# Kernel tuning notes

Measured on AMD Instinct MI355X. Metric: run time of the kernel, lower is better.

## Reference

```python
import jax, jax.numpy as jnp
import numpy as np

DIM = 2048
HEADS = 16
DIM_HEAD = 128
DIM_INNER = HEADS * DIM_HEAD
BATCH = 2
SEQ = 2048
EPS = 1e-12  # F.normalize default eps


def l2norm(t, axis=-1):
    # matches F.normalize(t, dim=axis, p=2): t / max(||t||, eps)
    n = jnp.sqrt(jnp.sum(t * t, axis=axis, keepdims=True))
    return t / jnp.maximum(n, EPS)


def setup_inputs() -> dict:
    key = jax.random.key(0)
    ks = jax.random.split(key, 5)
    x = jax.random.normal(ks[0], (BATCH, SEQ, DIM), dtype=jnp.float32)
    # NormLinear weights (torch Linear layout: [out, in]); parametrization
    # l2-normalizes rows (dim=-1) for q/k/v and columns (dim=0) for to_out.
    Wq = jax.random.normal(ks[1], (DIM_INNER, DIM), dtype=jnp.float32) / np.sqrt(DIM)
    Wk = jax.random.normal(ks[2], (DIM_INNER, DIM), dtype=jnp.float32) / np.sqrt(DIM)
    Wv = jax.random.normal(ks[3], (DIM_INNER, DIM), dtype=jnp.float32) / np.sqrt(DIM)
    Wout = jax.random.normal(ks[4], (DIM, DIM_INNER), dtype=jnp.float32) / np.sqrt(DIM_INNER)
    # Scale(dim_inner, init=1.0, scale=dim**-1): param = ones * dim**-1,
    # forward_scale = init/scale = dim, so qk_scale() starts at 1.0
    qk_scale = jnp.ones((DIM_INNER,), dtype=jnp.float32) / DIM
    return {"x": x, "Wq": Wq, "Wk": Wk, "Wv": Wv, "Wout": Wout, "qk_scale": qk_scale}


def reference(x, Wq, Wk, Wv, Wout, qk_scale):
    b, n, _ = x.shape
    # NormLinear: x @ l2norm(W, rows).T  (scale = groups**-1 = 1)
    q = jnp.einsum('bnd,ed->bne', x, l2norm(Wq, axis=-1))
    k = jnp.einsum('bnd,ed->bne', x, l2norm(Wk, axis=-1))
    v = jnp.einsum('bnd,ed->bne', x, l2norm(Wv, axis=-1))
    # split heads: b n (h d) -> b h n d
    split = lambda t: t.reshape(b, n, HEADS, DIM_HEAD).transpose(0, 2, 1, 3)
    q, k, v = split(q), split(k), split(v)
    # per-head l2norm of q and k over head dim
    q = l2norm(q, axis=-1)
    k = l2norm(k, axis=-1)
    # learned qk scale: (h d) -> h 1 d, effective = param * forward_scale(=DIM)
    q = q * (qk_scale * DIM).reshape(HEADS, 1, DIM_HEAD)
    # causal SDPA with scale = sqrt(dim_head) (unit-norm q,k in nGPT)
    attn_scale = DIM_HEAD ** 0.5
    scores = jnp.einsum('bhid,bhjd->bhij', q, k) * attn_scale
    causal = jnp.tril(jnp.ones((n, n), dtype=bool))
    scores = jnp.where(causal, scores, jnp.finfo(scores.dtype).min)
    attn = jax.nn.softmax(scores, axis=-1)
    out = jnp.einsum('bhij,bhjd->bhid', attn, v)
    # merge heads: b h n d -> b n (h d)
    out = out.transpose(0, 2, 1, 3).reshape(b, n, DIM_INNER)
    # to_out: NormLinear with norm over dim=0 of weight [DIM, DIM_INNER]
    out = jnp.einsum('bne,de->bnd', out, l2norm(Wout, axis=0))
    return out
```

## Files before the change

kernel.cpp:

```cpp
#include <hip/hip_runtime.h>


typedef __bf16 bf16x8 __attribute__((ext_vector_type(8)));
typedef float f32x4 __attribute__((ext_vector_type(4)));

__device__ __forceinline__ unsigned short f2bf(float f) {
  unsigned int u = __float_as_uint(f);
  u = u + 0x7FFFu + ((u >> 16) & 1u);
  return (unsigned short)(u >> 16);
}

__device__ __forceinline__ void async16(const void* g, void* l) {
  __builtin_amdgcn_global_load_lds(
      (const __attribute__((address_space(1))) unsigned int*)g,
      (__attribute__((address_space(3))) unsigned int*)l, 16, 0, 0);
}

#define QFOLD (2048.0f * 11.313708498984761f * 1.4426950408889634f)


__global__ __launch_bounds__(256) void prep_w_rows(
    const float* __restrict__ Wq, const float* __restrict__ Wk,
    const float* __restrict__ Wv, ushort* __restrict__ oq,
    ushort* __restrict__ ok_, ushort* __restrict__ ov) {
  const int row = blockIdx.x;
  const float* W = (blockIdx.y == 0) ? Wq : (blockIdx.y == 1) ? Wk : Wv;
  ushort* O = (blockIdx.y == 0) ? oq : (blockIdx.y == 1) ? ok_ : ov;
  const int t = threadIdx.x;
  const float4* Wr = (const float4*)(W + (size_t)row * 2048);
  float4 v0 = Wr[t];
  float4 v1 = Wr[t + 256];
  float ss = v0.x * v0.x + v0.y * v0.y + v0.z * v0.z + v0.w * v0.w +
             v1.x * v1.x + v1.y * v1.y + v1.z * v1.z + v1.w * v1.w;
  ss += __shfl_xor(ss, 1);  ss += __shfl_xor(ss, 2);
  ss += __shfl_xor(ss, 4);  ss += __shfl_xor(ss, 8);
  ss += __shfl_xor(ss, 16); ss += __shfl_xor(ss, 32);
  __shared__ float red[4];
  if ((t & 63) == 0) red[t >> 6] = ss;
  __syncthreads();
  float tot = red[0] + red[1] + red[2] + red[3];
  float sc = 1.0f / fmaxf(sqrtf(tot), 1e-12f);
  ushort4 o0, o1;
  o0.x = f2bf(v0.x * sc); o0.y = f2bf(v0.y * sc);
  o0.z = f2bf(v0.z * sc); o0.w = f2bf(v0.w * sc);
  o1.x = f2bf(v1.x * sc); o1.y = f2bf(v1.y * sc);
  o1.z = f2bf(v1.z * sc); o1.w = f2bf(v1.w * sc);
  *(ushort4*)(O + (size_t)row * 2048 + t * 4) = o0;
  *(ushort4*)(O + (size_t)row * 2048 + 1024 + t * 4) = o1;
}

__global__ __launch_bounds__(256) void wout_colss(const float* __restrict__ W,
                                                  float* __restrict__ colss) {
  const int e = blockIdx.x * 256 + threadIdx.x;
  const int d0 = blockIdx.y * 128;
  float ss = 0.f;
  #pragma unroll 8
  for (int i = 0; i < 128; ++i) {
    float v = W[(size_t)(d0 + i) * 2048 + e];
    ss += v * v;
  }
  atomicAdd(colss + e, ss);
}

__global__ __launch_bounds__(256) void wout_norm(const float* __restrict__ W,
                                                 const float* __restrict__ colss,
                                                 ushort* __restrict__ O) {
  const int idx = (blockIdx.x * 256 + threadIdx.x) * 4;
  float4 v = *(const float4*)(W + idx);
  float4 c = *(const float4*)(colss + (idx & 2047));
  ushort4 o;
  o.x = f2bf(v.x / fmaxf(sqrtf(c.x), 1e-12f));
  o.y = f2bf(v.y / fmaxf(sqrtf(c.y), 1e-12f));
  o.z = f2bf(v.z / fmaxf(sqrtf(c.z), 1e-12f));
  o.w = f2bf(v.w / fmaxf(sqrtf(c.w), 1e-12f));
  *(ushort4*)(O + idx) = o;
}

__global__ __launch_bounds__(256) void convert_x(const float* __restrict__ X,
                                                 ushort* __restrict__ O) {
  const int idx = (blockIdx.x * 256 + threadIdx.x) * 4;
  float4 v = *(const float4*)(X + idx);
  ushort4 o;
  o.x = f2bf(v.x); o.y = f2bf(v.y); o.z = f2bf(v.z); o.w = f2bf(v.w);
  *(ushort4*)(O + idx) = o;
}

__global__ __launch_bounds__(64) void qk_mhead(const float* __restrict__ qks,
                                               float* __restrict__ mh) {
  const int h = blockIdx.x, l = threadIdx.x;
  float m = fmaxf(fabsf(qks[h * 128 + l]), fabsf(qks[h * 128 + 64 + l]));
  m = fmaxf(m, __shfl_xor(m, 1));  m = fmaxf(m, __shfl_xor(m, 2));
  m = fmaxf(m, __shfl_xor(m, 4));  m = fmaxf(m, __shfl_xor(m, 8));
  m = fmaxf(m, __shfl_xor(m, 16)); m = fmaxf(m, __shfl_xor(m, 32));
  if (l == 0) mh[h] = m * QFOLD;
}


#define LDSBUF 49152
#define ABYTES 32768

__device__ __forceinline__ void mainloop_256x128(
    const ushort* __restrict__ A, const ushort* __restrict__ Bw,
    int m0, int n0, char* lds, f32x4 acc[4][4], int t) {
  const int l = t & 63, w = t >> 6;
  const int wm = w & 3, wn = w >> 2;
  const int l15 = l & 15, l4 = l >> 4;

  const int lc = (t & 7) ^ ((t >> 3) & 7);
  const ushort* srcA = A + (size_t)m0 * 2048 + (t >> 3) * 2048 + lc * 8;
  const ushort* srcB = Bw + (size_t)n0 * 2048 + (t >> 3) * 2048 + lc * 8;
  char* dstA = lds + t * 16;
  char* dstB = lds + ABYTES + t * 16;

  const int rdA = (wm * 64 + l15) * 128;
  const int rdB = ABYTES + (wn * 64 + l15) * 128;
  const int cb0 = ((l4 ^ (l15 & 7)) * 16);
  const int cb1 = (((4 + l4) ^ (l15 & 7)) * 16);

  auto stageA = [&](int s, int k0, int o) {
    async16(srcA + (size_t)o * 131072 + k0, dstA + s * LDSBUF + o * 8192);
  };
  auto stageB = [&](int s, int k0, int o) {
    async16(srcB + (size_t)o * 131072 + k0, dstB + s * LDSBUF + o * 8192);
  };

  #pragma unroll
  for (int i = 0; i < 4; ++i)
    #pragma unroll
    for (int j = 0; j < 4; ++j) acc[i][j] = (f32x4){0.f, 0.f, 0.f, 0.f};

  stageA(0, 0, 0); stageA(0, 0, 1); stageA(0, 0, 2); stageA(0, 0, 3);
  stageB(0, 0, 0); stageB(0, 0, 1);
  stageA(1, 64, 0); stageA(1, 64, 1); stageA(1, 64, 2); stageA(1, 64, 3);
  stageB(1, 64, 0); stageB(1, 64, 1);
  asm volatile("s_waitcnt vmcnt(6)" ::: "memory");
  __builtin_amdgcn_s_barrier();

  auto tile = [&](int s, int s2, int k2, bool pf) {
    const char* Ab = lds + s * LDSBUF;
    bf16x8 af[4][2], bg[4][2];
    #pragma unroll
    for (int fm = 0; fm < 4; ++fm) {
      af[fm][0] = *(const bf16x8*)(Ab + rdA + fm * 2048 + cb0);
      af[fm][1] = *(const bf16x8*)(Ab + rdA + fm * 2048 + cb1);
    }
    #pragma unroll
    for (int fn = 0; fn < 2; ++fn) {
      bg[fn][0] = *(const bf16x8*)(Ab + rdB + fn * 2048 + cb0);
      bg[fn][1] = *(const bf16x8*)(Ab + rdB + fn * 2048 + cb1);
    }
    if (pf) { stageA(s2, k2, 0); stageA(s2, k2, 1); stageA(s2, k2, 2); }
    __builtin_amdgcn_s_setprio(1);
    #pragma unroll
    for (int ks = 0; ks < 2; ++ks)
      #pragma unroll
      for (int fm = 0; fm < 4; ++fm)
        #pragma unroll
        for (int fn = 0; fn < 2; ++fn)
          acc[fm][fn] = __builtin_amdgcn_mfma_f32_16x16x32_bf16(
              af[fm][ks], bg[fn][ks], acc[fm][fn], 0, 0, 0);
    __builtin_amdgcn_s_setprio(0);
    #pragma unroll
    for (int fn = 2; fn < 4; ++fn) {
      bg[fn][0] = *(const bf16x8*)(Ab + rdB + fn * 2048 + cb0);
      bg[fn][1] = *(const bf16x8*)(Ab + rdB + fn * 2048 + cb1);
    }
    if (pf) { stageA(s2, k2, 3); stageB(s2, k2, 0); stageB(s2, k2, 1); }
    __builtin_amdgcn_s_setprio(1);
    #pragma unroll
    for (int ks = 0; ks < 2; ++ks)
      #pragma unroll
      for (int fm = 0; fm < 4; ++fm)
        #pragma unroll
        for (int fn = 2; fn < 4; ++fn)
          acc[fm][fn] = __builtin_amdgcn_mfma_f32_16x16x32_bf16(
              af[fm][ks], bg[fn][ks], acc[fm][fn], 0, 0, 0);
    __builtin_amdgcn_s_setprio(0);
  };

  #pragma unroll 1
  for (int kt = 0; kt < 30; kt += 3) {
    tile(0, 2, (kt + 2) * 64, true);
    asm volatile("s_waitcnt vmcnt(6)" ::: "memory");
    __builtin_amdgcn_s_barrier();
    tile(1, 0, (kt + 3) * 64, true);
    asm volatile("s_waitcnt vmcnt(6)" ::: "memory");
    __builtin_amdgcn_s_barrier();
    tile(2, 1, (kt + 4) * 64, true);
    asm volatile("s_waitcnt vmcnt(6)" ::: "memory");
    __builtin_amdgcn_s_barrier();
  }
  tile(0, 0, 0, false);
  asm volatile("s_waitcnt vmcnt(0)" ::: "memory");
  __builtin_amdgcn_s_barrier();
  tile(1, 0, 0, false);
}

__global__ __launch_bounds__(512, 2) void gemm_qkv(
    const ushort* __restrict__ X, const ushort* __restrict__ Wq,
    const ushort* __restrict__ Wk, const ushort* __restrict__ Wv,
    const float* __restrict__ qks, ushort* __restrict__ qn,
    ushort* __restrict__ kn, ushort* __restrict__ vt) {
  __shared__ __align__(16) char lds[3 * LDSBUF];
  __shared__ float partials[2][256];
  const int z = blockIdx.z;
  const ushort* Bw = (z == 0) ? Wq : (z == 1) ? Wk : Wv;
  const int n0 = blockIdx.x * 128;
  const int m0 = blockIdx.y * 256;
  const int t = threadIdx.x;
  const int l = t & 63, w = t >> 6;
  const int wm = w & 3, wn = w >> 2;
  const int l15 = l & 15, l4 = l >> 4;

  f32x4 acc[4][4];
  mainloop_256x128(X, Bw, m0, n0, lds, acc, t);

  const int h = blockIdx.x;
  if (z == 2) {
    const int bb = m0 >> 11, nb = m0 & 2047;
    #pragma unroll
    for (int fm = 0; fm < 4; ++fm) {
      int nn = nb + wm * 64 + fm * 16 + l4 * 4;
      #pragma unroll
      for (int fn = 0; fn < 4; ++fn) {
        int d = wn * 64 + fn * 16 + l15;
        ushort4 p;
        p.x = f2bf(acc[fm][fn][0]); p.y = f2bf(acc[fm][fn][1]);
        p.z = f2bf(acc[fm][fn][2]); p.w = f2bf(acc[fm][fn][3]);
        *(ushort4*)(vt + (size_t)((bb * 16 + h) * 128 + d) * 2048 + nn) = p;
      }
    }
  } else {
    #pragma unroll
    for (int fm = 0; fm < 4; ++fm)
      #pragma unroll
      for (int r = 0; r < 4; ++r) {
        float s = 0.f;
        #pragma unroll
        for (int fn = 0; fn < 4; ++fn) {
          float v = acc[fm][fn][r];
          s += v * v;
        }
        s += __shfl_xor(s, 1); s += __shfl_xor(s, 2);
        s += __shfl_xor(s, 4); s += __shfl_xor(s, 8);
        if (l15 == 0) partials[wn][wm * 64 + fm * 16 + l4 * 4 + r] = s;
      }
    __syncthreads();
    float cs[4];
    #pragma unroll
    for (int fn = 0; fn < 4; ++fn)
      cs[fn] = (z == 0) ? qks[n0 + wn * 64 + fn * 16 + l15] * QFOLD : 1.0f;
    ushort* O = (z == 0) ? qn : kn;
    #pragma unroll
    for (int fm = 0; fm < 4; ++fm)
      #pragma unroll
      for (int r = 0; r < 4; ++r) {
        int i = wm * 64 + fm * 16 + l4 * 4 + r;
        float tot = partials[0][i] + partials[1][i];
        float sc = 1.0f / fmaxf(sqrtf(tot), 1e-12f);
        #pragma unroll
        for (int fn = 0; fn < 4; ++fn)
          O[(size_t)(m0 + i) * 2048 + n0 + wn * 64 + fn * 16 + l15] =
              f2bf(acc[fm][fn][r] * sc * cs[fn]);
      }
  }
}

__global__ __launch_bounds__(256, 3) void attn_kernel(
    const ushort* __restrict__ qn, const ushort* __restrict__ kn,
    const ushort* __restrict__ vt, const float* __restrict__ mhead,
    ushort* __restrict__ ao) {
  const int hb = blockIdx.x;
  const int b = hb >> 4, h = hb & 15;
  const int qt = 31 - blockIdx.y;
  const int i0 = qt * 64;
  const int t = threadIdx.x, w = t >> 6, l = t & 63;
  const int l15 = l & 15, l4 = l >> 4;

  __shared__ __align__(16) ushort Ks[64 * 136];
  __shared__ __align__(16) ushort Vts[128 * 72];
  __shared__ __align__(16) ushort Ps[64 * 72];

  bf16x8 qf[4];
  #pragma unroll
  for (int ks = 0; ks < 4; ++ks)
    qf[ks] = *(const bf16x8*)(qn +
        (size_t)(b * 2048 + i0 + w * 16 + l15) * 2048 +
        h * 128 + ks * 32 + l4 * 8);

  f32x4 Oa[8];
  #pragma unroll
  for (int fd = 0; fd < 8; ++fd) Oa[fd] = (f32x4){0.f, 0.f, 0.f, 0.f};
  f32x4 Ol = (f32x4){0.f, 0.f, 0.f, 0.f};

  const float mh = mhead[h];
  const __bf16 one = (__bf16)1.0f;
  const bf16x8 ones = {one, one, one, one, one, one, one, one};

  const ushort* kbase = kn + (size_t)(b * 2048) * 2048 + h * 128;
  const ushort* vbase = vt + (size_t)((b * 16 + h) * 128) * 2048;

  for (int jt = 0; jt <= qt; ++jt) {
    const int j0 = jt * 64;
    __syncthreads();
    #pragma unroll
    for (int pass = 0; pass < 5; ++pass) {
      int c = pass * 256 + t;
      if (c < 1088) {
        int r = c / 17, dc = c - r * 17;
        int dcc = (dc == 16) ? 0 : dc;
        async16(kbase + (size_t)(j0 + r) * 2048 + dcc * 8, (char*)Ks + c * 16);
      }
    }
    #pragma unroll
    for (int pass = 0; pass < 5; ++pass) {
      int c = pass * 256 + t;
      if (c < 1152) {
        int r = c / 9, jc = c - r * 9;
        int jcc = (jc == 8) ? 0 : jc;
        async16(vbase + (size_t)r * 2048 + j0 + jcc * 8, (char*)Vts + c * 16);
      }
    }
    __syncthreads();

    f32x4 Sa[4];
    #pragma unroll
    for (int fj = 0; fj < 4; ++fj) {
      f32x4 s0 = (f32x4){0.f, 0.f, 0.f, 0.f};
      #pragma unroll
      for (int ks = 0; ks < 4; ++ks) {
        bf16x8 kf = *(const bf16x8*)&Ks[(fj * 16 + l15) * 136 + ks * 32 + l4 * 8];
        s0 = __builtin_amdgcn_mfma_f32_16x16x32_bf16(qf[ks], kf, s0, 0, 0, 0);
      }
      Sa[fj] = s0;
    }

    if (jt == qt) {
      #pragma unroll
      for (int fj = 0; fj < 4; ++fj)
        #pragma unroll
        for (int r = 0; r < 4; ++r) {
          int jg = fj * 16 + l15;
          int ig = w * 16 + l4 * 4 + r;
          if (jg > ig) Sa[fj][r] = -1e30f;
        }
    }

    #pragma unroll
    for (int fj = 0; fj < 4; ++fj)
      #pragma unroll
      for (int r = 0; r < 4; ++r)
        Ps[(w * 16 + l4 * 4 + r) * 72 + fj * 16 + l15] =
            f2bf(__builtin_exp2f(Sa[fj][r] - mh));

    #pragma unroll
    for (int ks = 0; ks < 2; ++ks) {
      bf16x8 p0 = *(const bf16x8*)&Ps[(w * 16 + l15) * 72 + ks * 32 + l4 * 8];
      Ol = __builtin_amdgcn_mfma_f32_16x16x32_bf16(p0, ones, Ol, 0, 0, 0);
      #pragma unroll
      for (int fd = 0; fd < 8; ++fd) {
        bf16x8 vf = *(const bf16x8*)&Vts[(fd * 16 + l15) * 72 + ks * 32 + l4 * 8];
        Oa[fd] = __builtin_amdgcn_mfma_f32_16x16x32_bf16(p0, vf, Oa[fd], 0, 0, 0);
      }
    }
  }

  #pragma unroll
  for (int r = 0; r < 4; ++r) {
    float inv = 1.0f / Ol[r];
    int ig = i0 + w * 16 + l4 * 4 + r;
    #pragma unroll
    for (int fd = 0; fd < 8; ++fd)
      ao[(size_t)(b * 2048 + ig) * 2048 + h * 128 + fd * 16 + l15] =
          f2bf(Oa[fd][r] * inv);
  }
}

__global__ __launch_bounds__(512, 2) void gemm_out(
    const ushort* __restrict__ A, const ushort* __restrict__ Bw,
    float* __restrict__ C) {
  __shared__ __align__(16) char lds[3 * LDSBUF];
  const int n0 = blockIdx.x * 128;
  const int m0 = blockIdx.y * 256;
  const int t = threadIdx.x;
  const int l = t & 63, w = t >> 6;
  const int wm = w & 3, wn = w >> 2;
  const int l15 = l & 15, l4 = l >> 4;

  f32x4 acc[4][4];
  mainloop_256x128(A, Bw, m0, n0, lds, acc, t);

  #pragma unroll
  for (int fm = 0; fm < 4; ++fm)
    #pragma unroll
    for (int fn = 0; fn < 4; ++fn)
      #pragma unroll
      for (int r = 0; r < 4; ++r)
        C[(size_t)(m0 + wm * 64 + fm * 16 + l4 * 4 + r) * 2048 +
          n0 + wn * 64 + fn * 16 + l15] = acc[fm][fn][r];
}

extern "C" void kernel_launch(void* const* d_in, const int* in_sizes, int n_in,
                              void* d_out, int out_size, void* d_ws, size_t ws_size,
                              hipStream_t stream) {
  (void)in_sizes; (void)n_in; (void)out_size; (void)ws_size;
  const float* x    = (const float*)d_in[0];
  const float* Wq   = (const float*)d_in[1];
  const float* Wk   = (const float*)d_in[2];
  const float* Wv   = (const float*)d_in[3];
  const float* Wout = (const float*)d_in[4];
  const float* qks  = (const float*)d_in[5];
  char* ws = (char*)d_ws;

  ushort* wqn  = (ushort*)(ws + 0);
  ushort* wkn  = (ushort*)(ws + 8388608);
  ushort* wvn  = (ushort*)(ws + 16777216);
  ushort* wotn = (ushort*)(ws + 25165824);
  ushort* xbf  = (ushort*)(ws + 33554432);
  ushort* qn   = (ushort*)(ws + 50331648);
  ushort* kn   = (ushort*)(ws + 67108864);
  ushort* vt   = (ushort*)(ws + 83886080);
  ushort* ao   = (ushort*)(ws + 100663296);
  float* colss = (float*)(ws + 117440512);
  float* mh    = (float*)(ws + 117448704);
  float* out   = (float*)d_out;

  hipMemsetAsync(colss, 0, 2048 * sizeof(float), stream);
  prep_w_rows<<<dim3(2048, 3), 256, 0, stream>>>(Wq, Wk, Wv, wqn, wkn, wvn);
  wout_colss<<<dim3(8, 16), 256, 0, stream>>>(Wout, colss);
  wout_norm<<<4096, 256, 0, stream>>>(Wout, colss, wotn);
  convert_x<<<8192, 256, 0, stream>>>(x, xbf);
  qk_mhead<<<16, 64, 0, stream>>>(qks, mh);
  gemm_qkv<<<dim3(16, 16, 3), 512, 0, stream>>>(xbf, wqn, wkn, wvn, qks, qn, kn, vt);
  attn_kernel<<<dim3(32, 32), 256, 0, stream>>>(qn, kn, vt, mh, ao);
  gemm_out<<<dim3(16, 16), 512, 0, stream>>>(ao, wotn, out);
}
```

Baseline: 376.5 us.

## Fuse prep kernels and swap QKV GEMM to single-buffered 128x128 tiles

Four small launches are merged into one branching prep_all kernel: the memset, the row normalization of Wq/Wk/Wv, the bf16 conversion of x and the per-head qk max. This removes launch and serialization overhead. The QKV projection GEMM drops the triple-buffered, software-pipelined 256x128 mainloop. It now uses a simple single-buffered 128x128 tile with 256 threads, padded LDS rows and two barriers per k-step, relying on higher occupancy (4 blocks per CU) for latency hiding. This gives up overlap of global loads with MFMA work in exchange for more resident blocks and smaller tiles.

```diff
diff --git a/kernel.cpp b/kernel.cpp
--- a/kernel.cpp
+++ b/kernel.cpp
@@ -18,35 +18,60 @@
 
 #define QFOLD (2048.0f * 11.313708498984761f * 1.4426950408889634f)
 
-
-__global__ __launch_bounds__(256) void prep_w_rows(
-    const float* __restrict__ Wq, const float* __restrict__ Wk,
-    const float* __restrict__ Wv, ushort* __restrict__ oq,
-    ushort* __restrict__ ok_, ushort* __restrict__ ov) {
-  const int row = blockIdx.x;
-  const float* W = (blockIdx.y == 0) ? Wq : (blockIdx.y == 1) ? Wk : Wv;
-  ushort* O = (blockIdx.y == 0) ? oq : (blockIdx.y == 1) ? ok_ : ov;
+__global__ __launch_bounds__(256) void prep_all(
+    const float* __restrict__ x, const float* __restrict__ Wq,
+    const float* __restrict__ Wk, const float* __restrict__ Wv,
+    const float* __restrict__ qks, ushort* __restrict__ xbf,
+    ushort* __restrict__ wqn, ushort* __restrict__ wkn,
+    ushort* __restrict__ wvn, float* __restrict__ colss,
+    float* __restrict__ mh) {
+  const int bid = blockIdx.x;
   const int t = threadIdx.x;
-  const float4* Wr = (const float4*)(W + (size_t)row * 2048);
-  float4 v0 = Wr[t];
-  float4 v1 = Wr[t + 256];
-  float ss = v0.x * v0.x + v0.y * v0.y + v0.z * v0.z + v0.w * v0.w +
-             v1.x * v1.x + v1.y * v1.y + v1.z * v1.z + v1.w * v1.w;
-  ss += __shfl_xor(ss, 1);  ss += __shfl_xor(ss, 2);
-  ss += __shfl_xor(ss, 4);  ss += __shfl_xor(ss, 8);
-  ss += __shfl_xor(ss, 16); ss += __shfl_xor(ss, 32);
-  __shared__ float red[4];
-  if ((t & 63) == 0) red[t >> 6] = ss;
-  __syncthreads();
-  float tot = red[0] + red[1] + red[2] + red[3];
-  float sc = 1.0f / fmaxf(sqrtf(tot), 1e-12f);
-  ushort4 o0, o1;
-  o0.x = f2bf(v0.x * sc); o0.y = f2bf(v0.y * sc);
-  o0.z = f2bf(v0.z * sc); o0.w = f2bf(v0.w * sc);
-  o1.x = f2bf(v1.x * sc); o1.y = f2bf(v1.y * sc);
-  o1.z = f2bf(v1.z * sc); o1.w = f2bf(v1.w * sc);
-  *(ushort4*)(O + (size_t)row * 2048 + t * 4) = o0;
-  *(ushort4*)(O + (size_t)row * 2048 + 1024 + t * 4) = o1;
+  if (bid < 6144) {
+    const int z = bid >> 11, row = bid & 2047;
+    const float* W = (z == 0) ? Wq : (z == 1) ? Wk : Wv;
+    ushort* O = (z == 0) ? wqn : (z == 1) ? wkn : wvn;
+    const float4* Wr = (const float4*)(W + (size_t)row * 2048);
+    float4 v0 = Wr[t];
+    float4 v1 = Wr[t + 256];
+    float ss = v0.x * v0.x + v0.y * v0.y + v0.z * v0.z + v0.w * v0.w +
+               v1.x * v1.x + v1.y * v1.y + v1.z * v1.z + v1.w * v1.w;
+    ss += __shfl_xor(ss, 1);  ss += __shfl_xor(ss, 2);
+    ss += __shfl_xor(ss, 4);  ss += __shfl_xor(ss, 8);
+    ss += __shfl_xor(ss, 16); ss += __shfl_xor(ss, 32);
+    __shared__ float red[4];
+    if ((t & 63) == 0) red[t >> 6] = ss;
+    __syncthreads();
+    float tot = red[0] + red[1] + red[2] + red[3];
+    float sc = 1.0f / fmaxf(sqrtf(tot), 1e-12f);
+    ushort4 o0, o1;
+    o0.x = f2bf(v0.x * sc); o0.y = f2bf(v0.y * sc);
+    o0.z = f2bf(v0.z * sc); o0.w = f2bf(v0.w * sc);
+    o1.x = f2bf(v1.x * sc); o1.y = f2bf(v1.y * sc);
+    o1.z = f2bf(v1.z * sc); o1.w = f2bf(v1.w * sc);
+    *(ushort4*)(O + (size_t)row * 2048 + t * 4) = o0;
+    *(ushort4*)(O + (size_t)row * 2048 + 1024 + t * 4) = o1;
+  } else if (bid < 14336) {
+    const int idx = ((bid - 6144) * 256 + t) * 4;
+    float4 v = *(const float4*)(x + idx);
+    ushort4 o;
+    o.x = f2bf(v.x); o.y = f2bf(v.y); o.z = f2bf(v.z); o.w = f2bf(v.w);
+    *(ushort4*)(xbf + idx) = o;
+  } else if (bid < 14352) {
+    const int h = bid - 14336;
+    if (t < 64) {
+      const int l = t;
+      float m = fmaxf(fabsf(qks[h * 128 + l]), fabsf(qks[h * 128 + 64 + l]));
+      m = fmaxf(m, __shfl_xor(m, 1));  m = fmaxf(m, __shfl_xor(m, 2));
+      m = fmaxf(m, __shfl_xor(m, 4));  m = fmaxf(m, __shfl_xor(m, 8));
+      m = fmaxf(m, __shfl_xor(m, 16)); m = fmaxf(m, __shfl_xor(m, 32));
+      if (l == 0) mh[h] = m * QFOLD;
+    }
+  } else {
+    float4 z4 = (float4){0.f, 0.f, 0.f, 0.f};
+    ((float4*)colss)[t] = z4;
+    ((float4*)colss)[t + 256] = z4;
+  }
 }
 
 __global__ __launch_bounds__(256) void wout_colss(const float* __restrict__ W,
@@ -76,23 +101,129 @@
   *(ushort4*)(O + idx) = o;
 }
 
-__global__ __launch_bounds__(256) void convert_x(const float* __restrict__ X,
-                                                 ushort* __restrict__ O) {
-  const int idx = (blockIdx.x * 256 + threadIdx.x) * 4;
-  float4 v = *(const float4*)(X + idx);
-  ushort4 o;
-  o.x = f2bf(v.x); o.y = f2bf(v.y); o.z = f2bf(v.z); o.w = f2bf(v.w);
-  *(ushort4*)(O + idx) = o;
-}
-
-__global__ __launch_bounds__(64) void qk_mhead(const float* __restrict__ qks,
-                                               float* __restrict__ mh) {
-  const int h = blockIdx.x, l = threadIdx.x;
-  float m = fmaxf(fabsf(qks[h * 128 + l]), fabsf(qks[h * 128 + 64 + l]));
-  m = fmaxf(m, __shfl_xor(m, 1));  m = fmaxf(m, __shfl_xor(m, 2));
-  m = fmaxf(m, __shfl_xor(m, 4));  m = fmaxf(m, __shfl_xor(m, 8));
-  m = fmaxf(m, __shfl_xor(m, 16)); m = fmaxf(m, __shfl_xor(m, 32));
-  if (l == 0) mh[h] = m * QFOLD;
+__device__ __forceinline__ void gemm_mainloop(
+    const ushort* __restrict__ A, const ushort* __restrict__ Bw,
+    int m0, int n0, ushort* As, ushort* Bs, f32x4 acc[4][4],
+    int t, int l, int wm, int wn) {
+  const int l15 = l & 15, l4 = l >> 4;
+  const ushort* abase = A + (size_t)m0 * 2048;
+  const ushort* bbase = Bw + (size_t)n0 * 2048;
+  for (int kt = 0; kt < 32; ++kt) {
+    const int k0 = kt * 64;
+    __syncthreads();
+    #pragma unroll
+    for (int p = 0; p < 9; ++p) {
+      int c = p * 256 + t;
+      const ushort* src = abase;
+      char* dst = (char*)As;
+      int cc = c;
+      if (c >= 1152) { cc = c - 1152; src = bbase; dst = (char*)Bs; }
+      int r = cc / 9, dc = cc - r * 9;
+      int dcc = (dc == 8) ? 0 : dc;
+      async16(src + (size_t)r * 2048 + k0 + dcc * 8, dst + cc * 16);
+    }
+    __syncthreads();
+    #pragma unroll
+    for (int ks = 0; ks < 2; ++ks) {
+      bf16x8 af[4], bg[4];
+      #pragma unroll
+      for (int f = 0; f < 4; ++f)
+        af[f] = *(const bf16x8*)&As[(wm * 64 + f * 16 + l15) * 72 + ks * 32 + l4 * 8];
+      #pragma unroll
+      for (int f = 0; f < 4; ++f)
+        bg[f] = *(const bf16x8*)&Bs[(wn * 64 + f * 16 + l15) * 72 + ks * 32 + l4 * 8];
+      #pragma unroll
+      for (int fm = 0; fm < 4; ++fm)
+        #pragma unroll
+        for (int fn = 0; fn < 4; ++fn)
+          acc[fm][fn] = __builtin_amdgcn_mfma_f32_16x16x32_bf16(
+              af[fm], bg[fn], acc[fm][fn], 0, 0, 0);
+    }
+  }
+}
+
+__global__ __launch_bounds__(256, 4) void gemm_qkv(
+    const ushort* __restrict__ X, const ushort* __restrict__ Wq,
+    const ushort* __restrict__ Wk, const ushort* __restrict__ Wv,
+    const float* __restrict__ qks, ushort* __restrict__ qn,
+    ushort* __restrict__ kn, ushort* __restrict__ vt) {
+  const int z = blockIdx.z;
+  const ushort* Bw = (z == 0) ? Wq : (z == 1) ? Wk : Wv;
+  const int n0 = blockIdx.x * 128;
+  const int m0 = blockIdx.y * 128;
+  __shared__ __align__(16) ushort As[128 * 72];
+  __shared__ __align__(16) ushort Bs[128 * 72];
+  __shared__ float partials[2][128];
+  const int t = threadIdx.x, w = t >> 6, l = t & 63;
+  const int wm = w & 1, wn = w >> 1;
+  const int l15 = l & 15, l4 = l >> 4;
+
+  f32x4 acc[4][4];
+  #pragma unroll
+  for (int i = 0; i < 4; ++i)
+    #pragma unroll
+    for (int j = 0; j < 4; ++j) acc[i][j] = (f32x4){0.f, 0.f, 0.f, 0.f};
+
+  gemm_mainloop(X, Bw, m0, n0, As, Bs, acc, t, l, wm, wn);
+
+  const int h = n0 >> 7;
+  if (z == 2) {
+    #pragma unroll
+    for (int fm = 0; fm < 4; ++fm) {
+      int mrow = m0 + wm * 64 + fm * 16 + l4 * 4;
+      int bb = mrow >> 11;
+      int nn = mrow & 2047;
+      #pragma unroll
+      for (int fn = 0; fn < 4; ++fn) {
+        int d = wn * 64 + fn * 16 + l15;
+        ushort4 p;
+        p.x = f2bf(acc[fm][fn][0]); p.y = f2bf(acc[fm][fn][1]);
+        p.z = f2bf(acc[fm][fn][2]); p.w = f2bf(acc[fm][fn][3]);
+        *(ushort4*)(vt + (size_t)((bb * 16 + h) * 128 + d) * 2048 + nn) = p;
+      }
+    }
+  } else {
+    float rs[4][4];
+    #pragma unroll
+    for (int fm = 0; fm < 4; ++fm)
+      #pragma unroll
+      for (int r = 0; r < 4; ++r) {
+        float s = 0.f;
+        #pragma unroll
+        for (int fn = 0; fn < 4; ++fn) {
+          float v = acc[fm][fn][r];
+          s += v * v;
+        }
+        s += __shfl_xor(s, 1); s += __shfl_xor(s, 2);
+        s += __shfl_xor(s, 4); s += __shfl_xor(s, 8);
+        rs[fm][r] = s;
+      }
+    if (l15 == 0) {
+      #pragma unroll
+      for (int fm = 0; fm < 4; ++fm)
+        #pragma unroll
+        for (int r = 0; r < 4; ++r)
+          partials[wn][wm * 64 + fm * 16 + l4 * 4 + r] = rs[fm][r];
+    }
+    __syncthreads();
+    float cs[4];
+    #pragma unroll
+    for (int fn = 0; fn < 4; ++fn)
+      cs[fn] = (z == 0) ? qks[n0 + wn * 64 + fn * 16 + l15] * QFOLD : 1.0f;
+    ushort* O = (z == 0) ? qn : kn;
+    #pragma unroll
+    for (int fm = 0; fm < 4; ++fm)
+      #pragma unroll
+      for (int r = 0; r < 4; ++r) {
+        int i = wm * 64 + fm * 16 + l4 * 4 + r;
+        float tot = partials[0][i] + partials[1][i];
+        float sc = 1.0f / fmaxf(sqrtf(tot), 1e-12f);
+        #pragma unroll
+        for (int fn = 0; fn < 4; ++fn)
+          O[(size_t)(m0 + i) * 2048 + n0 + wn * 64 + fn * 16 + l15] =
+              f2bf(acc[fm][fn][r] * sc * cs[fn]);
+      }
+  }
 }
 
 
@@ -194,76 +325,6 @@
   asm volatile("s_waitcnt vmcnt(0)" ::: "memory");
   __builtin_amdgcn_s_barrier();
   tile(1, 0, 0, false);
-}
-
-__global__ __launch_bounds__(512, 2) void gemm_qkv(
-    const ushort* __restrict__ X, const ushort* __restrict__ Wq,
-    const ushort* __restrict__ Wk, const ushort* __restrict__ Wv,
-    const float* __restrict__ qks, ushort* __restrict__ qn,
-    ushort* __restrict__ kn, ushort* __restrict__ vt) {
-  __shared__ __align__(16) char lds[3 * LDSBUF];
-  __shared__ float partials[2][256];
-  const int z = blockIdx.z;
-  const ushort* Bw = (z == 0) ? Wq : (z == 1) ? Wk : Wv;
-  const int n0 = blockIdx.x * 128;
-  const int m0 = blockIdx.y * 256;
-  const int t = threadIdx.x;
-  const int l = t & 63, w = t >> 6;
-  const int wm = w & 3, wn = w >> 2;
-  const int l15 = l & 15, l4 = l >> 4;
-
-  f32x4 acc[4][4];
-  mainloop_256x128(X, Bw, m0, n0, lds, acc, t);
-
-  const int h = blockIdx.x;
-  if (z == 2) {
-    const int bb = m0 >> 11, nb = m0 & 2047;
-    #pragma unroll
-    for (int fm = 0; fm < 4; ++fm) {
-      int nn = nb + wm * 64 + fm * 16 + l4 * 4;
-      #pragma unroll
-      for (int fn = 0; fn < 4; ++fn) {
-        int d = wn * 64 + fn * 16 + l15;
-        ushort4 p;
-        p.x = f2bf(acc[fm][fn][0]); p.y = f2bf(acc[fm][fn][1]);
-        p.z = f2bf(acc[fm][fn][2]); p.w = f2bf(acc[fm][fn][3]);
-        *(ushort4*)(vt + (size_t)((bb * 16 + h) * 128 + d) * 2048 + nn) = p;
-      }
-    }
-  } else {
-    #pragma unroll
-    for (int fm = 0; fm < 4; ++fm)
-      #pragma unroll
-      for (int r = 0; r < 4; ++r) {
-        float s = 0.f;
-        #pragma unroll
-        for (int fn = 0; fn < 4; ++fn) {
-          float v = acc[fm][fn][r];
-          s += v * v;
-        }
-        s += __shfl_xor(s, 1); s += __shfl_xor(s, 2);
-        s += __shfl_xor(s, 4); s += __shfl_xor(s, 8);
-        if (l15 == 0) partials[wn][wm * 64 + fm * 16 + l4 * 4 + r] = s;
-      }
-    __syncthreads();
-    float cs[4];
-    #pragma unroll
-    for (int fn = 0; fn < 4; ++fn)
-      cs[fn] = (z == 0) ? qks[n0 + wn * 64 + fn * 16 + l15] * QFOLD : 1.0f;
-    ushort* O = (z == 0) ? qn : kn;
-    #pragma unroll
-    for (int fm = 0; fm < 4; ++fm)
-      #pragma unroll
-      for (int r = 0; r < 4; ++r) {
-        int i = wm * 64 + fm * 16 + l4 * 4 + r;
-        float tot = partials[0][i] + partials[1][i];
-        float sc = 1.0f / fmaxf(sqrtf(tot), 1e-12f);
-        #pragma unroll
-        for (int fn = 0; fn < 4; ++fn)
-          O[(size_t)(m0 + i) * 2048 + n0 + wn * 64 + fn * 16 + l15] =
-              f2bf(acc[fm][fn][r] * sc * cs[fn]);
-      }
-  }
 }
 
 __global__ __launch_bounds__(256, 3) void attn_kernel(
@@ -425,13 +486,11 @@
   float* mh    = (float*)(ws + 117448704);
   float* out   = (float*)d_out;
 
-  hipMemsetAsync(colss, 0, 2048 * sizeof(float), stream);
-  prep_w_rows<<<dim3(2048, 3), 256, 0, stream>>>(Wq, Wk, Wv, wqn, wkn, wvn);
+  prep_all<<<14353, 256, 0, stream>>>(x, Wq, Wk, Wv, qks, xbf, wqn, wkn, wvn,
+                                      colss, mh);
   wout_colss<<<dim3(8, 16), 256, 0, stream>>>(Wout, colss);
   wout_norm<<<4096, 256, 0, stream>>>(Wout, colss, wotn);
-  convert_x<<<8192, 256, 0, stream>>>(x, xbf);
-  qk_mhead<<<16, 64, 0, stream>>>(qks, mh);
-  gemm_qkv<<<dim3(16, 16, 3), 512, 0, stream>>>(xbf, wqn, wkn, wvn, qks, qn, kn, vt);
+  gemm_qkv<<<dim3(16, 32, 3), 256, 0, stream>>>(xbf, wqn, wkn, wvn, qks, qn, kn, vt);
   attn_kernel<<<dim3(32, 32), 256, 0, stream>>>(qn, kn, vt, mh, ao);
   gemm_out<<<dim3(16, 16), 512, 0, stream>>>(ao, wotn, out);
 }
```

After: 372.4 us. About the same (-1.1%).
